# Optimization experiments

Measured on AMD Instinct MI355X. Metric: run time of the kernel, lower is better.

Reference implementation:

```python
import jax, jax.numpy as jnp
import numpy as np

N, E, DIM, H = 50000, 800000, 64, 2
HD = H * DIM


def setup_inputs() -> dict:
    key = jax.random.key(0)
    ks = jax.random.split(key, 16)
    s = 0.05
    return {
        "x": jax.random.normal(ks[0], (N, DIM), jnp.float32),
        "edge_index": jax.random.randint(ks[1], (2, E), 0, N, jnp.int64),
        "Wq": jax.random.normal(ks[2], (DIM, HD), jnp.float32) * s,
        "bq": jax.random.normal(ks[3], (HD,), jnp.float32) * s,
        "Wk": jax.random.normal(ks[4], (DIM, HD), jnp.float32) * s,
        "bk": jax.random.normal(ks[5], (HD,), jnp.float32) * s,
        "Wv": jax.random.normal(ks[6], (DIM, HD), jnp.float32) * s,
        "bv": jax.random.normal(ks[7], (HD,), jnp.float32) * s,
        "Wskip": jax.random.normal(ks[8], (DIM, HD), jnp.float32) * s,
        "bskip": jax.random.normal(ks[9], (HD,), jnp.float32) * s,
        "Wc": jax.random.normal(ks[10], (HD, DIM), jnp.float32) * s,
        "bc": jax.random.normal(ks[11], (DIM,), jnp.float32) * s,
        "gamma": jnp.ones((DIM,), jnp.float32),
        "beta": jnp.zeros((DIM,), jnp.float32),
    }


def reference(x, edge_index, Wq, bq, Wk, bk, Wv, bv, Wskip, bskip, Wc, bc, gamma, beta):
    src, dst = edge_index[0], edge_index[1]  # messages flow src -> dst
    # TransformerConv: per-head q/k/v projections, [N, H, D]
    q = (x @ Wq + bq).reshape(N, H, DIM)
    k = (x @ Wk + bk).reshape(N, H, DIM)
    v = (x @ Wv + bv).reshape(N, H, DIM)
    scale = 1.0 / np.sqrt(DIM).astype(np.float32)
    # edge-wise attention logits: [E, H]
    alpha = jnp.einsum('ehd,ehd->eh', q[dst], k[src]) * scale
    # segment softmax over incoming edges of each dst node (PyG softmax)
    amax = jax.ops.segment_max(alpha, dst, num_segments=N)
    a = jnp.exp(alpha - amax[dst])
    asum = jax.ops.segment_sum(a, dst, num_segments=N)
    a = a / (asum[dst] + 1e-16)
    # weighted scatter-aggregate of values: [N, H, D] -> concat heads
    out = jax.ops.segment_sum(a[:, :, None] * v[src], dst, num_segments=N)
    out = out.reshape(N, HD)
    # root/skip connection (root_weight=True default)
    out = out + (x @ Wskip + bskip)
    # concat linear: H*D -> dim
    out = out @ Wc + bc
    # pyg.LayerNorm default mode='graph': normalize over ALL nodes+features
    out = out - out.mean()
    out = out / (out.std() + 1e-5)  # std with unbiased=False (jnp default ddof=0)
    return out * gamma + beta
```

## Files before the change

kernel.cpp:

```cpp
#include <hip/hip_runtime.h>
#include <hip/hip_bf16.h>

#define N_NODES 50000
#define N_EDGES 800000
#define DIM 64
#define NHEAD 2
#define HD 128
#define NCOL 448
#define MAXDEG 64

#define NBIN 196
#define BCAP 6144
#define ACH 2048
#define BIN_BLKS 391

#define PREP_B 112
#define PROJ_B 782
#define ATTN_B 1563

#define QSCALE 0.18033688011112042f

typedef short bf16x8 __attribute__((ext_vector_type(8)));
typedef float f32x16 __attribute__((ext_vector_type(16)));
typedef float f32x2 __attribute__((ext_vector_type(2)));

__device__ __forceinline__ unsigned short f2bf(float f) {
    unsigned u = __float_as_uint(f);
    unsigned r = (u + 0x7fffu + ((u >> 16) & 1u)) >> 16;
    return (unsigned short)r;
}
__device__ __forceinline__ unsigned char f2fp8(float f) {
    int r = __builtin_amdgcn_cvt_pk_fp8_f32(f, f, 0, false);
    return (unsigned char)(r & 0xff);
}

__global__ __launch_bounds__(256) void k_pb(
    const int* __restrict__ ei,
    const float* __restrict__ Wq, const float* __restrict__ bq,
    const float* __restrict__ Wk, const float* __restrict__ bk,
    const float* __restrict__ Wv, const float* __restrict__ bv,
    const float* __restrict__ Wskip, const float* __restrict__ bskip,
    const float* __restrict__ Wc, const float* __restrict__ bc,
    unsigned short* __restrict__ WallT, float* __restrict__ ball,
    int* __restrict__ bincnt, unsigned* __restrict__ bins,
    double* __restrict__ sacc)
{
    const int t = threadIdx.x;
    if (blockIdx.x < PREP_B) {
        if (blockIdx.x == 0) { sacc[t] = 0.0; sacc[256 + t] = 0.0; }
        int gid = blockIdx.x * 256 + t;
        const int j = gid >> 6;
        const int d = gid & 63;
        float w, bb;
        if (j < 128) {
            w = Wq[d * HD + j] * QSCALE;
            bb = bq[j] * QSCALE;
        } else if (j < 256) {
            int jj = j - 128;
            w = Wk[d * HD + jj];
            bb = bk[jj];
        } else if (j < 384) {
            int jj = j - 256;
            int h = jj >> 6, jc = jj & 63;
            float s = 0.f, sb = 0.f;
            for (int c = 0; c < 64; c++) {
                float wc = Wc[(h * 64 + c) * DIM + jc];
                s  += Wv[d * HD + h * 64 + c] * wc;
                sb += bv[h * 64 + c] * wc;
            }
            w = s; bb = sb;
        } else {
            int jj = j - 384;
            float s = 0.f, sb = bc[jj];
            for (int c = 0; c < HD; c++) {
                float wc = Wc[c * DIM + jj];
                s  += Wskip[d * HD + c] * wc;
                sb += bskip[c] * wc;
            }
            w = s; bb = sb;
        }
        WallT[gid] = f2bf(w);
        if (d == 0) ball[j] = bb;
        return;
    }
    __shared__ int hist[256];
    __shared__ int gbase[256];
    const int e0 = (blockIdx.x - PREP_B) * ACH;
    hist[t] = 0;
    __syncthreads();
    unsigned pk8[8];
    int bin8[8], sl8[8];
#pragma unroll
    for (int k = 0; k < 8; k++) {
        int e = e0 + t + k * 256;
        if (e < N_EDGES) {
            int src = ei[e];
            int d = ei[N_EDGES + e];
            int bin = d >> 8;
            pk8[k] = (unsigned)(((d & 255) << 16) | src);
            bin8[k] = bin;
            sl8[k] = atomicAdd(&hist[bin], 1);
        } else {
            bin8[k] = -1;
        }
    }
    __syncthreads();
    if (t < NBIN) {
        int h = hist[t];
        if (h > 0) gbase[t] = atomicAdd(&bincnt[t], h);
    }
    __syncthreads();
#pragma unroll
    for (int k = 0; k < 8; k++) {
        int bin = bin8[k];
        if (bin >= 0) {
            int pos = gbase[bin] + sl8[k];
            if (pos < BCAP) bins[(size_t)bin * BCAP + pos] = pk8[k];
        }
    }
}

__global__ __launch_bounds__(256) void k_ep(
    const float* __restrict__ x,
    const unsigned short* __restrict__ WallT, const float* __restrict__ ball,
    float* __restrict__ q, unsigned char* __restrict__ kv, float* __restrict__ skipc,
    const int* __restrict__ bincnt, const unsigned* __restrict__ bins,
    int* __restrict__ deg, unsigned short* __restrict__ elist)
{
    __shared__ __align__(16) unsigned char smem[65536];
    const int blk = blockIdx.x;
    const int t = threadIdx.x;
    if (blk >= PROJ_B) {
        const int bin = blk - PROJ_B;
        int* nodecnt = (int*)smem;
        nodecnt[t] = 0;
        __syncthreads();
        int cnt = bincnt[bin]; if (cnt > BCAP) cnt = BCAP;
        const unsigned* bp = bins + (size_t)bin * BCAP;
        for (int i = t; i < cnt; i += 256) {
            unsigned p = bp[i];
            int local = p >> 16;
            int src = p & 0xffff;
            int sl = atomicAdd(&nodecnt[local], 1);
            if (sl < MAXDEG)
                elist[((size_t)((bin << 8) | local)) * MAXDEG + sl] = (unsigned short)src;
        }
        __syncthreads();
        int node = (bin << 8) + t;
        if (node < N_NODES) {
            int dgv = nodecnt[t];
            deg[node] = dgv > MAXDEG ? MAXDEG : dgv;
        }
        return;
    }
    float* q_s = (float*)smem;
    unsigned char* kv_s = smem + 32768;
    float* sk_s = (float*)(smem + 49152);

    const int w = t >> 6;
    const int lane = t & 63;
    const int col = lane & 31;
    const int khalf = lane >> 5;
    const int nloc0 = (w >> 1) * 32;
    const int n0 = blk * 64 + nloc0;
    const int ct0 = (w & 1) * 7;
    const int rowbase = 4 * khalf;

    int nread = n0 + col; if (nread >= N_NODES) nread = N_NODES - 1;
    const float* ap = x + (size_t)nread * 64 + khalf * 8;
    bf16x8 afrag[4];
#pragma unroll
    for (int kk = 0; kk < 4; kk++) {
        float4 xa = *((const float4*)(ap + kk * 16));
        float4 xb4 = *((const float4*)(ap + kk * 16 + 4));
        bf16x8 f;
        f[0] = (short)f2bf(xa.x); f[1] = (short)f2bf(xa.y);
        f[2] = (short)f2bf(xa.z); f[3] = (short)f2bf(xa.w);
        f[4] = (short)f2bf(xb4.x); f[5] = (short)f2bf(xb4.y);
        f[6] = (short)f2bf(xb4.z); f[7] = (short)f2bf(xb4.w);
        afrag[kk] = f;
    }

    for (int tt = 0; tt < 7; tt++) {
        const int gc = (ct0 + tt) * 32 + col;
        const float b = ball[gc];
        f32x16 acc;
#pragma unroll
        for (int r = 0; r < 16; r++) acc[r] = b;
        const unsigned short* bp = WallT + (size_t)gc * 64 + khalf * 8;
#pragma unroll
        for (int kk = 0; kk < 4; kk++) {
            bf16x8 bfrag = *((const bf16x8*)(bp + kk * 16));
            acc = __builtin_amdgcn_mfma_f32_32x32x16_bf16(afrag[kk], bfrag, acc, 0, 0, 0);
        }
        if (gc < 128) {
#pragma unroll
            for (int r = 0; r < 16; r++) {
                int nl = nloc0 + rowbase + (r & 3) + 8 * (r >> 2);
                q_s[nl * 128 + gc] = acc[r];
            }
        } else if (gc < 384) {
            int ch = gc - 128;
            int half = ch >> 7;
            int cc = ch & 127;
            int h = cc >> 6, c = cc & 63;
            int pos = half * 128 + ((c >> 3) << 4) + (h << 3) + (c & 7);
#pragma unroll
            for (int r = 0; r < 16; r++) {
                int nl = nloc0 + rowbase + (r & 3) + 8 * (r >> 2);
                kv_s[nl * 256 + pos] = f2fp8(acc[r]);
            }
        } else {
            int c = gc - 384;
#pragma unroll
            for (int r = 0; r < 16; r++) {
                int nl = nloc0 + rowbase + (r & 3) + 8 * (r >> 2);
                sk_s[nl * 64 + c] = acc[r];
            }
        }
    }
    __syncthreads();
    const size_t nbase = (size_t)blk * 64;
    const int nrem = (int)(N_NODES - nbase);
    {
        const float4* s4 = (const float4*)q_s;
        float4* g4 = (float4*)(q + nbase * HD);
        int lim = nrem >= 64 ? 2048 : nrem * 32;
#pragma unroll
        for (int kk = 0; kk < 8; kk++) {
            int i = t + kk * 256;
            if (i < lim) g4[i] = s4[i];
        }
    }
    {
        const uint4* s4 = (const uint4*)kv_s;
        uint4* g4 = (uint4*)(kv + nbase * 256);
        int lim = nrem >= 64 ? 1024 : nrem * 16;
#pragma unroll
        for (int kk = 0; kk < 4; kk++) {
            int i = t + kk * 256;
            if (i < lim) g4[i] = s4[i];
        }
    }
    {
        const float4* s4 = (const float4*)sk_s;
        float4* g4 = (float4*)(skipc + nbase * DIM);
        int lim = nrem >= 64 ? 1024 : nrem * 16;
#pragma unroll
        for (int kk = 0; kk < 4; kk++) {
            int i = t + kk * 256;
            if (i < lim) g4[i] = s4[i];
        }
    }
}

__global__ __launch_bounds__(256) void k_attn(
    const float* __restrict__ q, const unsigned char* __restrict__ kv,
    const float* __restrict__ skipc,
    const int* __restrict__ deg, const unsigned short* __restrict__ elist,
    float* __restrict__ out, double* __restrict__ sacc)
{
    const int w = threadIdx.x >> 6;
    const int lane = threadIdx.x & 63;
    const int g = lane >> 3;
    const int j = lane & 7;
    const int n = blockIdx.x * 32 + w * 8 + g;
    const bool nvalid = n < N_NODES;
    const int nn = nvalid ? n : N_NODES - 1;

    const uint4 E = *((const uint4*)(elist + (size_t)nn * MAXDEG + j * 8));
    int dg = nvalid ? deg[nn] : 0;
    if (dg > MAXDEG) dg = MAXDEG;
    int dgmax = dg;
#pragma unroll
    for (int off = 8; off < 64; off <<= 1) {
        int o = __shfl_xor(dgmax, off, 64);
        dgmax = o > dgmax ? o : dgmax;
    }

    const float4* qp4 = (const float4*)(q + (size_t)nn * HD);
    const float4 qa = qp4[2 * j],      qb = qp4[2 * j + 1];
    const float4 qc = qp4[16 + 2 * j], qd = qp4[17 + 2 * j];
    f32x2 q0[4], q1[4];
    q0[0] = (f32x2){qa.x, qa.y}; q0[1] = (f32x2){qa.z, qa.w};
    q0[2] = (f32x2){qb.x, qb.y}; q0[3] = (f32x2){qb.z, qb.w};
    q1[0] = (f32x2){qc.x, qc.y}; q1[1] = (f32x2){qc.z, qc.w};
    q1[2] = (f32x2){qd.x, qd.y}; q1[3] = (f32x2){qd.z, qd.w};

    f32x2 acc0[4], acc1[4];
#pragma unroll
    for (int i = 0; i < 4; i++) {
        acc0[i] = (f32x2){0.f, 0.f};
        acc1[i] = (f32x2){0.f, 0.f};
    }
    float l0 = 0.f, l1 = 0.f;

    for (int k = 0; k < dgmax; ++k) {
        const bool valid = k < dg;
        const int hw = k & 7;
        unsigned dwd = (hw < 4) ? ((hw < 2) ? E.x : E.y)
                                : ((hw < 6) ? E.z : E.w);
        unsigned v16 = (hw & 1) ? (dwd >> 16) : (dwd & 0xffffu);
        int s = __shfl((int)v16, (lane & 56) | (k >> 3), 64);
        if (!valid) s = 0;
        const uint4* kp = (const uint4*)(kv + (size_t)s * 256);
        const uint4 K = kp[j];
        const uint4 V = kp[8 + j];
        f32x2 p0v = q0[0] * __builtin_amdgcn_cvt_pk_f32_fp8(K.x, false);
        p0v += q0[1] * __builtin_amdgcn_cvt_pk_f32_fp8(K.x, true);
        p0v += q0[2] * __builtin_amdgcn_cvt_pk_f32_fp8(K.y, false);
        p0v += q0[3] * __builtin_amdgcn_cvt_pk_f32_fp8(K.y, true);
        f32x2 p1v = q1[0] * __builtin_amdgcn_cvt_pk_f32_fp8(K.z, false);
        p1v += q1[1] * __builtin_amdgcn_cvt_pk_f32_fp8(K.z, true);
        p1v += q1[2] * __builtin_amdgcn_cvt_pk_f32_fp8(K.w, false);
        p1v += q1[3] * __builtin_amdgcn_cvt_pk_f32_fp8(K.w, true);
        float p0 = p0v[0] + p0v[1];
        float p1 = p1v[0] + p1v[1];
#pragma unroll
        for (int off = 1; off < 8; off <<= 1) {
            p0 += __shfl_xor(p0, off, 64);
            p1 += __shfl_xor(p1, off, 64);
        }
        float w0 = valid ? __builtin_amdgcn_exp2f(p0) : 0.f;
        float w1 = valid ? __builtin_amdgcn_exp2f(p1) : 0.f;
        l0 += w0; l1 += w1;
        f32x2 w0v = {w0, w0}, w1v = {w1, w1};
        acc0[0] += w0v * __builtin_amdgcn_cvt_pk_f32_fp8(V.x, false);
        acc0[1] += w0v * __builtin_amdgcn_cvt_pk_f32_fp8(V.x, true);
        acc0[2] += w0v * __builtin_amdgcn_cvt_pk_f32_fp8(V.y, false);
        acc0[3] += w0v * __builtin_amdgcn_cvt_pk_f32_fp8(V.y, true);
        acc1[0] += w1v * __builtin_amdgcn_cvt_pk_f32_fp8(V.z, false);
        acc1[1] += w1v * __builtin_amdgcn_cvt_pk_f32_fp8(V.z, true);
        acc1[2] += w1v * __builtin_amdgcn_cvt_pk_f32_fp8(V.w, false);
        acc1[3] += w1v * __builtin_amdgcn_cvt_pk_f32_fp8(V.w, true);
    }

    const float inv0 = 1.f / (l0 + 1e-16f), inv1 = 1.f / (l1 + 1e-16f);
    const float4* sk = (const float4*)(skipc + (size_t)nn * DIM);
    const float4 sa = sk[2 * j], sb = sk[2 * j + 1];
    float* a0 = (float*)acc0;
    float* a1 = (float*)acc1;
    float o[8];
    o[0] = a0[0] * inv0 + a1[0] * inv1 + sa.x;
    o[1] = a0[1] * inv0 + a1[1] * inv1 + sa.y;
    o[2] = a0[2] * inv0 + a1[2] * inv1 + sa.z;
    o[3] = a0[3] * inv0 + a1[3] * inv1 + sa.w;
    o[4] = a0[4] * inv0 + a1[4] * inv1 + sb.x;
    o[5] = a0[5] * inv0 + a1[5] * inv1 + sb.y;
    o[6] = a0[6] * inv0 + a1[6] * inv1 + sb.z;
    o[7] = a0[7] * inv0 + a1[7] * inv1 + sb.w;
    if (nvalid) {
        float4 r0 = {o[0], o[1], o[2], o[3]}, r1 = {o[4], o[5], o[6], o[7]};
        float4* op = (float4*)(out + (size_t)n * DIM);
        op[2 * j] = r0; op[2 * j + 1] = r1;
    }
    float s_ = 0.f, ss = 0.f;
    if (nvalid) {
#pragma unroll
        for (int i = 0; i < 8; i++) { s_ += o[i]; ss += o[i] * o[i]; }
    }
#pragma unroll
    for (int off = 1; off < 64; off <<= 1) {
        s_ += __shfl_xor(s_, off, 64);
        ss += __shfl_xor(ss, off, 64);
    }
    if (lane == 0) {
        int slot = (blockIdx.x * 4 + w) & 255;
        atomicAdd(&sacc[slot], (double)s_);
        atomicAdd(&sacc[256 + slot], (double)ss);
    }
}

__global__ __launch_bounds__(256) void k_norm(
    float* __restrict__ out, const double* __restrict__ sacc,
    const float* __restrict__ gamma, const float* __restrict__ beta)
{
    const int t = threadIdx.x;
    __shared__ double red[8];
    double s = sacc[t];
    double ss = sacc[256 + t];
#pragma unroll
    for (int off = 32; off > 0; off >>= 1) {
        s  += __shfl_down(s, off);
        ss += __shfl_down(ss, off);
    }
    int wv = t >> 6;
    if ((t & 63) == 0) { red[wv * 2] = s; red[wv * 2 + 1] = ss; }
    __syncthreads();
    double S  = red[0] + red[2] + red[4] + red[6];
    double SS = red[1] + red[3] + red[5] + red[7];
    const double cnt = (double)N_NODES * (double)DIM;
    double mean = S / cnt;
    double var  = SS / cnt - mean * mean;
    if (var < 0.0) var = 0.0;
    float mf = (float)mean;
    float inv = 1.0f / ((float)sqrt(var) + 1e-5f);
    int i = blockIdx.x * 256 + t;
    if (i >= N_NODES * DIM / 4) return;
    float4 v = ((const float4*)out)[i];
    float4 gv = ((const float4*)gamma)[i & 15];
    float4 bv2 = ((const float4*)beta)[i & 15];
    v.x = (v.x - mf) * inv * gv.x + bv2.x;
    v.y = (v.y - mf) * inv * gv.y + bv2.y;
    v.z = (v.z - mf) * inv * gv.z + bv2.z;
    v.w = (v.w - mf) * inv * gv.w + bv2.w;
    ((float4*)out)[i] = v;
}

extern "C" void kernel_launch(void* const* d_in, const int* in_sizes, int n_in,
                              void* d_out, int out_size, void* d_ws, size_t ws_size,
                              hipStream_t stream) {
    const float* x     = (const float*)d_in[0];
    const int*   ei    = (const int*)d_in[1];
    const float* Wq    = (const float*)d_in[2];
    const float* bq    = (const float*)d_in[3];
    const float* Wk    = (const float*)d_in[4];
    const float* bk    = (const float*)d_in[5];
    const float* Wv    = (const float*)d_in[6];
    const float* bv    = (const float*)d_in[7];
    const float* Wsk   = (const float*)d_in[8];
    const float* bsk   = (const float*)d_in[9];
    const float* Wc    = (const float*)d_in[10];
    const float* bc    = (const float*)d_in[11];
    const float* gamma = (const float*)d_in[12];
    const float* beta  = (const float*)d_in[13];
    float* out = (float*)d_out;

    double* sacc = (double*)d_ws;
    float* ws = (float*)(sacc + 512);
    const size_t NF = (size_t)N_NODES * HD;
    float* q = ws;
    unsigned char* kv = (unsigned char*)(ws + NF);
    float* skipc = (float*)(kv + (size_t)N_NODES * 256);
    unsigned short* WallT = (unsigned short*)(skipc + (size_t)N_NODES * DIM);
    float* ball   = (float*)(WallT + NCOL * 64);
    int* bincnt   = (int*)(ball + NCOL);
    unsigned* bins = (unsigned*)(bincnt + 256);
    int* deg      = (int*)(bins + (size_t)NBIN * BCAP);
    unsigned short* elist = (unsigned short*)(deg + N_NODES);

    hipMemsetAsync(bincnt, 0, 256 * sizeof(int), stream);
    hipLaunchKernelGGL(k_pb, dim3(PREP_B + BIN_BLKS), dim3(256), 0, stream,
                       ei, Wq, bq, Wk, bk, Wv, bv, Wsk, bsk, Wc, bc,
                       WallT, ball, bincnt, bins, sacc);
    hipLaunchKernelGGL(k_ep, dim3(PROJ_B + NBIN), dim3(256), 0, stream,
                       x, WallT, ball, q, kv, skipc, bincnt, bins, deg, elist);
    hipLaunchKernelGGL(k_attn, dim3(ATTN_B), dim3(256), 0, stream,
                       q, kv, skipc, deg, elist, out, sacc);
    hipLaunchKernelGGL(k_norm, dim3(N_NODES * DIM / 4 / 256 + 1), dim3(256), 0, stream,
                       out, sacc, gamma, beta);
}
```

Before: 177.0 us.

## Split each node's edge loop across two 8-lane groups in attention kernel

The attention kernel now gives each destination node 16 lanes instead of 8. The two 8-lane halves process alternating incoming edges, and their partial softmax sums and accumulators are combined with a cross-lane shuffle at the end. This doubles the grid size and halves the serial edge-loop length per lane group, which exposes more parallel gather latency. The cost is an extra reduction step and lower lane utilisation for nodes whose degree is odd or small.

```diff
diff --git a/kernel.cpp b/kernel.cpp
--- a/kernel.cpp
+++ b/kernel.cpp
@@ -16,7 +16,7 @@
 
 #define PREP_B 112
 #define PROJ_B 782
-#define ATTN_B 1563
+#define ATTN_B 3125
 
 #define QSCALE 0.18033688011112042f
 
@@ -262,20 +262,19 @@
 {
     const int w = threadIdx.x >> 6;
     const int lane = threadIdx.x & 63;
-    const int g = lane >> 3;
+    const int e = (lane >> 3) & 1;
     const int j = lane & 7;
-    const int n = blockIdx.x * 32 + w * 8 + g;
+    const int n = blockIdx.x * 16 + w * 4 + (lane >> 4);
     const bool nvalid = n < N_NODES;
     const int nn = nvalid ? n : N_NODES - 1;
 
-    const uint4 E = *((const uint4*)(elist + (size_t)nn * MAXDEG + j * 8));
+    const uint2 E = *((const uint2*)(elist + (size_t)nn * MAXDEG + (lane & 15) * 4));
     int dg = nvalid ? deg[nn] : 0;
     if (dg > MAXDEG) dg = MAXDEG;
     int dgmax = dg;
-#pragma unroll
-    for (int off = 8; off < 64; off <<= 1) {
-        int o = __shfl_xor(dgmax, off, 64);
-        dgmax = o > dgmax ? o : dgmax;
+    {
+        int o1 = __shfl_xor(dgmax, 16, 64); if (o1 > dgmax) dgmax = o1;
+        int o2 = __shfl_xor(dgmax, 32, 64); if (o2 > dgmax) dgmax = o2;
     }
 
     const float4* qp4 = (const float4*)(q + (size_t)nn * HD);
@@ -295,14 +294,13 @@
     }
     float l0 = 0.f, l1 = 0.f;
 
-    for (int k = 0; k < dgmax; ++k) {
+    for (int b = 0; b < dgmax; b += 2) {
+        const int k = b + e;
         const bool valid = k < dg;
-        const int hw = k & 7;
-        unsigned dwd = (hw < 4) ? ((hw < 2) ? E.x : E.y)
-                                : ((hw < 6) ? E.z : E.w);
-        unsigned v16 = (hw & 1) ? (dwd >> 16) : (dwd & 0xffffu);
-        int s = __shfl((int)v16, (lane & 56) | (k >> 3), 64);
-        if (!valid) s = 0;
+        unsigned dwd = ((b >> 1) & 1) ? E.y : E.x;
+        int sd = __shfl((int)dwd, (lane & 48) | (b >> 2), 64);
+        unsigned v16 = e ? (((unsigned)sd) >> 16) : (((unsigned)sd) & 0xffffu);
+        int s = valid ? (int)v16 : 0;
         const uint4* kp = (const uint4*)(kv + (size_t)s * 256);
         const uint4 K = kp[j];
         const uint4 V = kp[8 + j];
@@ -335,29 +333,31 @@
         acc1[3] += w1v * __builtin_amdgcn_cvt_pk_f32_fp8(V.w, true);
     }
 
-    const float inv0 = 1.f / (l0 + 1e-16f), inv1 = 1.f / (l1 + 1e-16f);
-    const float4* sk = (const float4*)(skipc + (size_t)nn * DIM);
-    const float4 sa = sk[2 * j], sb = sk[2 * j + 1];
+    l0 += __shfl_xor(l0, 8, 64);
+    l1 += __shfl_xor(l1, 8, 64);
     float* a0 = (float*)acc0;
     float* a1 = (float*)acc1;
-    float o[8];
-    o[0] = a0[0] * inv0 + a1[0] * inv1 + sa.x;
-    o[1] = a0[1] * inv0 + a1[1] * inv1 + sa.y;
-    o[2] = a0[2] * inv0 + a1[2] * inv1 + sa.z;
-    o[3] = a0[3] * inv0 + a1[3] * inv1 + sa.w;
-    o[4] = a0[4] * inv0 + a1[4] * inv1 + sb.x;
-    o[5] = a0[5] * inv0 + a1[5] * inv1 + sb.y;
-    o[6] = a0[6] * inv0 + a1[6] * inv1 + sb.z;
-    o[7] = a0[7] * inv0 + a1[7] * inv1 + sb.w;
+#pragma unroll
+    for (int i = 0; i < 8; i++) {
+        a0[i] += __shfl_xor(a0[i], 8, 64);
+        a1[i] += __shfl_xor(a1[i], 8, 64);
+    }
+
+    const float inv0 = 1.f / (l0 + 1e-16f), inv1 = 1.f / (l1 + 1e-16f);
+    const float4 sk4 = ((const float4*)(skipc + (size_t)nn * DIM))[2 * j + e];
+    const int cb = e * 4;
+    float o0 = a0[cb + 0] * inv0 + a1[cb + 0] * inv1 + sk4.x;
+    float o1 = a0[cb + 1] * inv0 + a1[cb + 1] * inv1 + sk4.y;
+    float o2 = a0[cb + 2] * inv0 + a1[cb + 2] * inv1 + sk4.z;
+    float o3 = a0[cb + 3] * inv0 + a1[cb + 3] * inv1 + sk4.w;
     if (nvalid) {
-        float4 r0 = {o[0], o[1], o[2], o[3]}, r1 = {o[4], o[5], o[6], o[7]};
-        float4* op = (float4*)(out + (size_t)n * DIM);
-        op[2 * j] = r0; op[2 * j + 1] = r1;
+        float4 r = {o0, o1, o2, o3};
+        ((float4*)(out + (size_t)n * DIM))[2 * j + e] = r;
     }
     float s_ = 0.f, ss = 0.f;
     if (nvalid) {
-#pragma unroll
-        for (int i = 0; i < 8; i++) { s_ += o[i]; ss += o[i] * o[i]; }
+        s_ = o0 + o1 + o2 + o3;
+        ss = o0 * o0 + o1 * o1 + o2 * o2 + o3 * o3;
     }
 #pragma unroll
     for (int off = 1; off < 64; off <<= 1) {
```

After: 172.9 us. -2.3%, faster.
